# Kernel tuning notes

Hardware: AMD Instinct MI355X
Metric: run time of the kernel (lower is better)

Reference implementation:

```python
import jax, jax.numpy as jnp
import numpy as np

H = 8          # attention heads
D = 16         # per-head dim (hidden // heads)
HID = 128      # hidden_channels
OUT = 8        # out_channels of final linear
L = 2          # num_layers
NP = 100000    # num paper nodes
NA = 100000    # num author nodes
E = 500000     # edges per edge type
NEG_SLOPE = 0.2


def setup_inputs() -> dict:
    key = jax.random.key(0)
    ks = jax.random.split(key, 20)
    def nrm(k, shape, s=0.05):
        return jax.random.normal(k, shape, dtype=jnp.float32) * s
    return {
        'x_paper': jax.random.normal(ks[0], (NP, HID), dtype=jnp.float32),
        'x_author': jax.random.normal(ks[1], (NA, HID), dtype=jnp.float32),
        'Wp_p': nrm(ks[2], (L, HID, HID)),
        'bp_p': jnp.zeros((L, HID), jnp.float32),
        'Wp_a': nrm(ks[3], (L, HID, HID)),
        'bp_a': jnp.zeros((L, HID), jnp.float32),
        'as_ap': nrm(ks[4], (L, H, D), 0.2),
        'ad_ap': nrm(ks[5], (L, H, D), 0.2),
        'as_pa': nrm(ks[6], (L, H, D), 0.2),
        'ad_pa': nrm(ks[7], (L, H, D), 0.2),
        'as_pp': nrm(ks[8], (L, H, D), 0.2),
        'ad_pp': nrm(ks[9], (L, H, D), 0.2),
        'Wk': nrm(ks[10], (L, HID, HID)),
        'bk': jnp.zeros((L, HID), jnp.float32),
        'q': nrm(ks[11], (L, HID), 0.2),
        'Wout': nrm(ks[12], (HID, OUT)),
        'bout': jnp.zeros((OUT,), jnp.float32),
        'ei_ap': jax.random.randint(ks[13], (2, E), 0, NP, dtype=jnp.int32),
        'ei_pa': jax.random.randint(ks[14], (2, E), 0, NP, dtype=jnp.int32),
        'ei_pp': jax.random.randint(ks[15], (2, E), 0, NP, dtype=jnp.int32),
    }


def _leaky_relu(x):
    return jnp.where(x >= 0, x, NEG_SLOPE * x)


def _seg_softmax(alpha, dst, n):
    # PyG-style segment softmax over incoming edges of each dst node
    amax = jax.ops.segment_max(alpha, dst, num_segments=n)
    a = jnp.exp(alpha - amax[dst])
    denom = jax.ops.segment_sum(a, dst, num_segments=n) + 1e-16
    return a / denom[dst]


def _edge_attn_agg(z_src, z_dst, ei, a_s, a_d, n_dst):
    # per-edge-type GAT-style attention + scatter aggregate (HANConv message/aggregate)
    src, dst = ei[0], ei[1]
    alpha_src = (z_src * a_s).sum(-1)   # [Ns, H]
    alpha_dst = (z_dst * a_d).sum(-1)   # [Nd, H]
    alpha = _leaky_relu(alpha_src[src] + alpha_dst[dst])  # [E, H]
    alpha = _seg_softmax(alpha, dst, n_dst)
    msg = z_src[src] * alpha[:, :, None]                   # [E, H, D]
    out = jax.ops.segment_sum(msg, dst, num_segments=n_dst)
    return jax.nn.relu(out.reshape(n_dst, H * D))


def _group(outs, q, Wk, bk):
    # HANConv semantic-level attention across metapaths
    stacked = jnp.stack(outs)                               # [K, N, F]
    score = (q * jnp.tanh(stacked @ Wk + bk).mean(1)).sum(-1)  # [K]
    attn = jax.nn.softmax(score)
    return (attn[:, None, None] * stacked).sum(0)           # [N, F]


def _han_conv(xp, xa, ei_ap, ei_pa, ei_pp, Wp_p, bp_p, Wp_a, bp_a,
              as_ap, ad_ap, as_pa, ad_pa, as_pp, ad_pp, Wk, bk, q):
    zp = (xp @ Wp_p + bp_p).reshape(-1, H, D)
    za = (xa @ Wp_a + bp_a).reshape(-1, H, D)
    n_p, n_a = zp.shape[0], za.shape[0]
    out_ap = _edge_attn_agg(za, zp, ei_ap, as_ap, ad_ap, n_p)  # author -> paper
    out_pa = _edge_attn_agg(zp, za, ei_pa, as_pa, ad_pa, n_a)  # paper -> author
    out_pp = _edge_attn_agg(zp, zp, ei_pp, as_pp, ad_pp, n_p)  # paper -> paper
    new_xp = _group([out_ap, out_pp], q, Wk, bk)
    new_xa = _group([out_pa], q, Wk, bk)
    return new_xp, new_xa


def _forward(x_paper, x_author, Wp_p, bp_p, Wp_a, bp_a, as_ap, ad_ap,
             as_pa, ad_pa, as_pp, ad_pp, Wk, bk, q, Wout, bout,
             ei_ap, ei_pa, ei_pp):
    xp, xa = x_paper, x_author
    for l in range(L):
        xp, xa = _han_conv(xp, xa, ei_ap, ei_pa, ei_pp,
                           Wp_p[l], bp_p[l], Wp_a[l], bp_a[l],
                           as_ap[l], ad_ap[l], as_pa[l], ad_pa[l],
                           as_pp[l], ad_pp[l], Wk[l], bk[l], q[l])
        if l < L - 1:
            xp = jax.nn.elu(xp)  # dropout identity in eval mode (p applied only in training)
            xa = jax.nn.elu(xa)
    tgt = jax.nn.elu(xp)
    return tgt @ Wout + bout  # [NP, OUT]


def reference(x_paper, x_author, Wp_p, bp_p, Wp_a, bp_a, as_ap, ad_ap,
              as_pa, ad_pa, as_pp, ad_pp, Wk, bk, q, Wout, bout,
              ei_ap, ei_pa, ei_pp):
    return _forward(x_paper, x_author, Wp_p, bp_p, Wp_a, bp_a, as_ap, ad_ap,
                    as_pa, ad_pa, as_pp, ad_pp, Wk, bk, q, Wout, bout,
                    ei_ap, ei_pa, ei_pp)
```

## Files before the change

kernel.cpp:

```cpp
#include <hip/hip_runtime.h>

#define NHID 128
#define NHEAD 8
#define NNODE 100000
#define NEDGE 500000
#define NEG 0.2f
#define SCORE_GRID 512
#define GEMM_GRID 512
#define AGG_BLOCKS 12500
#define EB ((NEDGE + 255) / 256)
#define SB ((NNODE + 1023) / 1024)

typedef float4 f4;
typedef __attribute__((ext_vector_type(8))) short bfrag;
typedef __attribute__((ext_vector_type(4))) float facc;

__device__ inline float b2f(unsigned int u) {
    return __uint_as_float(u << 16);
}
__device__ inline unsigned short f2b(float f) {
    unsigned int u = __float_as_uint(f);
    unsigned int r = (u + 0x7FFFu + ((u >> 16) & 1u)) >> 16;
    return (unsigned short)r;
}
__device__ inline float fast_tanh(float x) {
    float e = __expf(2.f * x);
    return 1.f - 2.f / (e + 1.f);
}

struct WavSet {
    const float* W; const float* b;
    const float* v0; const float* v1; const float* v2; const float* v3;
    ushort* GT; float* bAv;
};

__global__ __launch_bounds__(256) void prep_fused(
    const float* __restrict__ w0, const float* __restrict__ w1,
    const float* __restrict__ w2, const float* __restrict__ w3,
    const float* __restrict__ w4, const float* __restrict__ w5,
    ushort* __restrict__ o0, ushort* __restrict__ o1,
    ushort* __restrict__ o2, ushort* __restrict__ o3,
    ushort* __restrict__ o4, ushort* __restrict__ o5,
    WavSet s0, WavSet s1, WavSet s2, WavSet s3,
    const int* __restrict__ e0, const int* __restrict__ e1,
    const int* __restrict__ e2, int* __restrict__ deg3)
{
    const int b = blockIdx.x;
    if (b < 384) {
        int which = b >> 6;
        int i = (b & 63) * 256 + threadIdx.x;
        const float* W = (which == 0) ? w0 : (which == 1) ? w1 : (which == 2) ? w2
                       : (which == 3) ? w3 : (which == 4) ? w4 : w5;
        ushort* Wt = (which == 0) ? o0 : (which == 1) ? o1 : (which == 2) ? o2
                   : (which == 3) ? o3 : (which == 4) ? o4 : o5;
        int fi = i >> 3, e = i & 7;
        int jk = fi >> 6, l = fi & 63;
        int j = jk >> 2, kk = jk & 3;
        int lr = l & 15, lg = l >> 4;
        Wt[i] = f2b(W[(kk * 32 + lg * 8 + e) * 128 + j * 16 + lr]);
    } else if (b < 448) {
        int bb = b - 384;
        int which = bb >> 4;
        const WavSet s = (which == 0) ? s0 : (which == 1) ? s1 : (which == 2) ? s2 : s3;
        int i = (bb & 15) * 256 + threadIdx.x;
        int fi = i >> 3, e = i & 7;
        int jk = fi >> 6, l = fi & 63;
        int jt = jk >> 2, kk = jk & 3;
        int lr = l & 15, lg = l >> 4;
        int c = jt * 16 + lr;
        int m = kk * 32 + lg * 8 + e;
        int vec = c >> 3, h = c & 7;
        const float* vp = (vec == 0) ? s.v0 : (vec == 1) ? s.v1 : (vec == 2) ? s.v2 : s.v3;
        float sv = 0.f;
        if (vp) {
            #pragma unroll
            for (int dd = 0; dd < 16; ++dd)
                sv = fmaf(s.W[m * 128 + h * 16 + dd], vp[h * 16 + dd], sv);
        }
        s.GT[i] = f2b(sv);
        if (i < 32) {
            int cc = i, vv = cc >> 3, hh = cc & 7;
            const float* vq = (vv == 0) ? s.v0 : (vv == 1) ? s.v1 : (vv == 2) ? s.v2 : s.v3;
            float t = 0.f;
            if (vq) {
                #pragma unroll
                for (int dd = 0; dd < 16; ++dd)
                    t = fmaf(s.b[hh * 16 + dd], vq[hh * 16 + dd], t);
            }
            s.bAv[cc] = t;
        }
    } else {
        int bb2 = b - 448;
        int ty = bb2 / EB, bb = bb2 % EB;
        const int* ei = (ty == 0) ? e0 : (ty == 1) ? e1 : e2;
        int e = bb * 256 + threadIdx.x;
        if (e < NEDGE) atomicAdd(deg3 + ty * NNODE + ei[NEDGE + e], 1);
    }
}

struct PArgs {
    const void* A;
    const ushort* A2;
    const ushort* WtT;
    const ushort* GT;
    const float* bias;
    const float* bAv;
    ushort* C;
    float* ao0; float* ao1; float* ao2; float* ao3;
    int mode;
};

template<int M0, int M1, int SCAT>
__global__ __launch_bounds__(256) void gemm_persist(
    PArgs g0, PArgs g1, const float* __restrict__ attn, int nt, int N,
    const int* __restrict__ e0, const int* __restrict__ e1,
    const int* __restrict__ e2, int* __restrict__ cur3, int* __restrict__ cols3)
{
    if (SCAT && blockIdx.x >= GEMM_GRID) {
        int bb2 = blockIdx.x - GEMM_GRID;
        int ty = bb2 / EB, bb = bb2 % EB;
        const int* ei = (ty == 0) ? e0 : (ty == 1) ? e1 : e2;
        int e = bb * 256 + threadIdx.x;
        if (e < NEDGE) {
            int d = ei[NEDGE + e];
            int pos = atomicAdd(cur3 + ty * NNODE + d, 1);
            cols3[ty * NEDGE + pos] = ei[e];
        }
        return;
    }

    __shared__ uint4 smem[2560];
    const int hg = GEMM_GRID >> 1;
    const int half = (blockIdx.x >= hg) ? 1 : 0;
    const PArgs ga = half ? g1 : g0;
    const int MODE = half ? M1 : M0;
    const int b0 = half ? blockIdx.x - hg : blockIdx.x;

    const int tid = threadIdx.x;
    const int l = tid & 63, w = tid >> 6;
    const int lr = l & 15, lg = l >> 4;

    {
        const uint4* ws = reinterpret_cast<const uint4*>(ga.WtT);
        const uint4* gs = reinterpret_cast<const uint4*>(ga.GT);
        #pragma unroll
        for (int i = 0; i < 8; ++i) smem[tid + i * 256] = ws[tid + i * 256];
        #pragma unroll
        for (int i = 0; i < 2; ++i) smem[2048 + tid + i * 256] = gs[tid + i * 256];
    }
    float a0 = 0.f, a1 = 0.f;
    if (MODE == 2) { a0 = attn[0]; a1 = attn[1]; }
    __syncthreads();
    const ushort* WtL = reinterpret_cast<const ushort*>(smem);
    const ushort* GL  = WtL + 16384;

    float bv[8];
    #pragma unroll
    for (int j = 0; j < 8; ++j) bv[j] = ga.bias[j * 16 + lr];
    float bA[2];
    #pragma unroll
    for (int jt = 0; jt < 2; ++jt) bA[jt] = ga.bAv[jt * 16 + lr];

    uint4 rawA[(M0 == 0 && M1 == 0) ? 8 : 16];

    auto load_raw = [&](int t) {
        const int rw0 = t * 128 + w * 32;
        #pragma unroll
        for (int i = 0; i < 2; ++i) {
            int r = rw0 + i * 16 + lr; r = (r < N) ? r : (N - 1);
            if (MODE == 1) {
                const float* ap = (const float*)ga.A + (size_t)r * 128 + lg * 8;
                #pragma unroll
                for (int kk = 0; kk < 4; ++kk) {
                    rawA[i * 8 + kk * 2]     = *reinterpret_cast<const uint4*>(ap + kk * 32);
                    rawA[i * 8 + kk * 2 + 1] = *reinterpret_cast<const uint4*>(ap + kk * 32 + 4);
                }
            } else {
                const ushort* ap = (const ushort*)ga.A + (size_t)r * 128 + lg * 8;
                #pragma unroll
                for (int kk = 0; kk < 4; ++kk)
                    rawA[i * 4 + kk] = *reinterpret_cast<const uint4*>(ap + kk * 32);
                if (MODE == 2) {
                    const ushort* ap2 = ga.A2 + (size_t)r * 128 + lg * 8;
                    #pragma unroll
                    for (int kk = 0; kk < 4; ++kk)
                        rawA[8 + i * 4 + kk] = *reinterpret_cast<const uint4*>(ap2 + kk * 32);
                }
            }
        }
    };

    if (b0 >= nt) return;
    load_raw(b0);

    for (int t = b0; t < nt; t += hg) {
        const int rw0 = t * 128 + w * 32;

        bfrag av_[2][4];
        #pragma unroll
        for (int i = 0; i < 2; ++i) {
            #pragma unroll
            for (int kk = 0; kk < 4; ++kk) {
                if (MODE == 0) {
                    av_[i][kk] = *reinterpret_cast<bfrag*>(&rawA[i * 4 + kk]);
                } else if (MODE == 1) {
                    uint4 u = rawA[i * 8 + kk * 2];
                    uint4 v = rawA[i * 8 + kk * 2 + 1];
                    bfrag fr;
                    fr[0] = (short)f2b(__uint_as_float(u.x));
                    fr[1] = (short)f2b(__uint_as_float(u.y));
                    fr[2] = (short)f2b(__uint_as_float(u.z));
                    fr[3] = (short)f2b(__uint_as_float(u.w));
                    fr[4] = (short)f2b(__uint_as_float(v.x));
                    fr[5] = (short)f2b(__uint_as_float(v.y));
                    fr[6] = (short)f2b(__uint_as_float(v.z));
                    fr[7] = (short)f2b(__uint_as_float(v.w));
                    av_[i][kk] = fr;
                } else {
                    uint4 ua = rawA[i * 4 + kk];
                    uint4 ub = rawA[8 + i * 4 + kk];
                    unsigned int aa[4] = {ua.x, ua.y, ua.z, ua.w};
                    unsigned int bb[4] = {ub.x, ub.y, ub.z, ub.w};
                    bfrag fr;
                    #pragma unroll
                    for (int q = 0; q < 4; ++q) {
                        float lo = a0 * b2f(aa[q] & 0xffffu) + a1 * b2f(bb[q] & 0xffffu);
                        float hi = a0 * b2f(aa[q] >> 16)     + a1 * b2f(bb[q] >> 16);
                        fr[q * 2]     = (short)f2b(lo);
                        fr[q * 2 + 1] = (short)f2b(hi);
                    }
                    av_[i][kk] = fr;
                }
            }
        }

        if (t + hg < nt) load_raw(t + hg);

        facc accC[2][8], accP[2][2];
        #pragma unroll
        for (int i = 0; i < 2; ++i) {
            #pragma unroll
            for (int j = 0; j < 8; ++j) accC[i][j] = (facc){0.f, 0.f, 0.f, 0.f};
            #pragma unroll
            for (int jt = 0; jt < 2; ++jt) accP[i][jt] = (facc){0.f, 0.f, 0.f, 0.f};
        }

        #pragma unroll
        for (int kk = 0; kk < 4; ++kk) {
            #pragma unroll
            for (int j = 0; j < 8; ++j) {
                bfrag bfr = *reinterpret_cast<const bfrag*>(WtL + ((j * 4 + kk) * 64 + l) * 8);
                #pragma unroll
                for (int i = 0; i < 2; ++i)
                    accC[i][j] = __builtin_amdgcn_mfma_f32_16x16x32_bf16(
                        av_[i][kk], bfr, accC[i][j], 0, 0, 0);
            }
            #pragma unroll
            for (int jt = 0; jt < 2; ++jt) {
                bfrag gfr = *reinterpret_cast<const bfrag*>(GL + ((jt * 4 + kk) * 64 + l) * 8);
                #pragma unroll
                for (int i = 0; i < 2; ++i)
                    accP[i][jt] = __builtin_amdgcn_mfma_f32_16x16x32_bf16(
                        av_[i][kk], gfr, accP[i][jt], 0, 0, 0);
            }
        }

        #pragma unroll
        for (int j = 0; j < 8; ++j) {
            #pragma unroll
            for (int i = 0; i < 2; ++i) {
                #pragma unroll
                for (int rr = 0; rr < 4; ++rr) {
                    int row = rw0 + i * 16 + lg * 4 + rr;
                    if (row < N)
                        ga.C[(size_t)row * 128 + j * 16 + lr] = f2b(accC[i][j][rr] + bv[j]);
                }
            }
        }

        #pragma unroll
        for (int jt = 0; jt < 2; ++jt) {
            int c = jt * 16 + lr;
            int vec = c >> 3, h = c & 7;
            float* ao = (vec == 0) ? ga.ao0 : (vec == 1) ? ga.ao1
                      : (vec == 2) ? ga.ao2 : ga.ao3;
            if (ao == nullptr) continue;
            #pragma unroll
            for (int i = 0; i < 2; ++i) {
                #pragma unroll
                for (int rr = 0; rr < 4; ++rr) {
                    int row = rw0 + i * 16 + lg * 4 + rr;
                    if (row < N) ao[row * 8 + h] = accP[i][jt][rr] + bA[jt];
                }
            }
        }
    }
}

__global__ __launch_bounds__(256) void score_persist(
    const ushort* __restrict__ A0, const ushort* __restrict__ A1,
    const ushort* __restrict__ WtT, const float* __restrict__ bias,
    float* __restrict__ part, int nt, int N)
{
    __shared__ uint4 smem[2048];
    __shared__ float sred[4][256];
    const int tid = threadIdx.x;
    const int l = tid & 63, w = tid >> 6;
    const int lr = l & 15, lg = l >> 4;

    {
        const uint4* ws = reinterpret_cast<const uint4*>(WtT);
        #pragma unroll
        for (int i = 0; i < 8; ++i) smem[tid + i * 256] = ws[tid + i * 256];
    }
    __syncthreads();
    const ushort* WtL = reinterpret_cast<const ushort*>(smem);

    float bv[8];
    #pragma unroll
    for (int j = 0; j < 8; ++j) bv[j] = bias[j * 16 + lr];

    float cs[2][8];
    #pragma unroll
    for (int h = 0; h < 2; ++h)
        #pragma unroll
        for (int j = 0; j < 8; ++j) cs[h][j] = 0.f;

    const int total = 2 * nt;
    for (int t = blockIdx.x; t < total; t += gridDim.x) {
        const int half = (t >= nt) ? 1 : 0;
        const ushort* A = half ? A1 : A0;
        const int bb = half ? t - nt : t;
        const int rw0 = bb * 128 + w * 32;

        bfrag av_[2][4];
        #pragma unroll
        for (int i = 0; i < 2; ++i) {
            int r = rw0 + i * 16 + lr; r = (r < N) ? r : (N - 1);
            const ushort* ap = A + (size_t)r * 128 + lg * 8;
            #pragma unroll
            for (int kk = 0; kk < 4; ++kk)
                av_[i][kk] = *reinterpret_cast<const bfrag*>(ap + kk * 32);
        }

        facc acc[2][8];
        #pragma unroll
        for (int i = 0; i < 2; ++i)
            #pragma unroll
            for (int j = 0; j < 8; ++j) acc[i][j] = (facc){0.f, 0.f, 0.f, 0.f};

        #pragma unroll
        for (int kk = 0; kk < 4; ++kk) {
            #pragma unroll
            for (int j = 0; j < 8; ++j) {
                bfrag bfr = *reinterpret_cast<const bfrag*>(WtL + ((j * 4 + kk) * 64 + l) * 8);
                #pragma unroll
                for (int i = 0; i < 2; ++i)
                    acc[i][j] = __builtin_amdgcn_mfma_f32_16x16x32_bf16(
                        av_[i][kk], bfr, acc[i][j], 0, 0, 0);
            }
        }

        #pragma unroll
        for (int j = 0; j < 8; ++j) {
            float s = 0.f;
            #pragma unroll
            for (int i = 0; i < 2; ++i) {
                #pragma unroll
                for (int r = 0; r < 4; ++r) {
                    int row = rw0 + i * 16 + lg * 4 + r;
                    if (row < N) s += fast_tanh(acc[i][j][r] + bv[j]);
                }
            }
            cs[half][j] += s;
        }
    }

    #pragma unroll
    for (int h = 0; h < 2; ++h)
        #pragma unroll
        for (int j = 0; j < 8; ++j) {
            float s = cs[h][j];
            s += __shfl_xor(s, 16, 64);
            s += __shfl_xor(s, 32, 64);
            if (lg == 0) sred[w][h * 128 + j * 16 + lr] = s;
        }
    __syncthreads();
    float tot = sred[0][tid] + sred[1][tid] + sred[2][tid] + sred[3][tid];
    part[(size_t)blockIdx.x * 256 + tid] = tot;
}

__global__ void attn_reduce(const float* __restrict__ part,
                            const float* __restrict__ qv,
                            float* __restrict__ attn, int nb)
{
    __shared__ float sm[256];
    int t = threadIdx.x;
    float s0 = 0.f, s1 = 0.f, s2 = 0.f, s3 = 0.f;
    for (int b = 0; b < nb; b += 4) {
        s0 += part[(size_t)b * 256 + t];
        s1 += part[(size_t)(b + 1) * 256 + t];
        s2 += part[(size_t)(b + 2) * 256 + t];
        s3 += part[(size_t)(b + 3) * 256 + t];
    }
    sm[t] = (s0 + s1 + s2 + s3) * qv[t & 127];
    __syncthreads();
    if (t == 0) {
        float a = 0.f, b = 0.f;
        for (int i = 0; i < 128; ++i) { a += sm[i]; b += sm[128 + i]; }
        a *= (1.0f / 100000.0f);
        b *= (1.0f / 100000.0f);
        float m = fmaxf(a, b);
        float ea = expf(a - m), eb = expf(b - m);
        float inv = 1.f / (ea + eb);
        attn[0] = ea * inv;
        attn[1] = eb * inv;
    }
}

__global__ __launch_bounds__(1024) void scan_block3(
    const int* __restrict__ deg3, int* __restrict__ offs3, int* __restrict__ bsum3)
{
    __shared__ int sd[1024];
    int ty = blockIdx.x / SB, bb = blockIdx.x % SB;
    const int* deg = deg3 + ty * NNODE;
    int* offs = offs3 + ty * (NNODE + 1);
    int t = threadIdx.x, i = bb * 1024 + t;
    int v = (i < NNODE) ? deg[i] : 0;
    sd[t] = v; __syncthreads();
    for (int o = 1; o < 1024; o <<= 1) {
        int x = (t >= o) ? sd[t - o] : 0;
        __syncthreads();
        sd[t] += x;
        __syncthreads();
    }
    if (i < NNODE) offs[i + 1] = sd[t];
    if (t == 1023) bsum3[ty * 128 + bb] = sd[t];
}

__global__ void scan_bsum3(const int* __restrict__ bsum3, int* __restrict__ boff3)
{
    int t = threadIdx.x;
    if (t < 3) {
        int run = 0;
        for (int b = 0; b < SB; ++b) { boff3[t * 128 + b] = run; run += bsum3[t * 128 + b]; }
    }
}

__global__ __launch_bounds__(1024) void scan_add3(
    int* __restrict__ offs3, const int* __restrict__ boff3, int* __restrict__ cur3)
{
    int ty = blockIdx.x / SB, bb = blockIdx.x % SB;
    int* offs = offs3 + ty * (NNODE + 1);
    int* cur = cur3 + ty * NNODE;
    int i = bb * 1024 + threadIdx.x;
    if (i == 0) { offs[0] = 0; cur[0] = 0; }
    if (i < NNODE) {
        int v = offs[i + 1] + boff3[ty * 128 + bb];
        offs[i + 1] = v;
        if (i + 1 < NNODE) cur[i + 1] = v;
    }
}

struct AggJob {
    const int* offs; const int* cols;
    const float* asrc; const float* adst;
    const ushort* z; ushort* out;
};

__global__ __launch_bounds__(256) void agg_multi(AggJob j0, AggJob j1, AggJob j2)
{
    int jb = blockIdx.x / AGG_BLOCKS;
    const AggJob jj = (jb == 0) ? j0 : (jb == 1) ? j1 : j2;
    int bb = blockIdx.x - jb * AGG_BLOCKS;
    int w = threadIdx.x >> 6;
    int lane = threadIdx.x & 63;
    int halfid = lane >> 5;
    int sl = lane & 31;
    int d = bb * 8 + w * 2 + halfid;
    int h = sl >> 2;
    float ad = jj.adst[d * 8 + h];
    int e0 = jj.offs[d], e1 = jj.offs[d + 1];
    float acc0 = 0.f, acc1 = 0.f, acc2 = 0.f, acc3 = 0.f, psum = 0.f;
    const ushort* zbase = jj.z + sl * 4;
    for (int base = e0; base < e1; base += 4) {
        int idx[4];
        #pragma unroll
        for (int i = 0; i < 4; ++i) {
            int ee = base + i;
            idx[i] = jj.cols[(ee < e1) ? ee : (e1 - 1)];
        }
        float xs[4];
        #pragma unroll
        for (int i = 0; i < 4; ++i) xs[i] = jj.asrc[idx[i] * 8 + h];
        uint2 zv[4];
        #pragma unroll
        for (int i = 0; i < 4; ++i)
            zv[i] = *reinterpret_cast<const uint2*>(zbase + (size_t)idx[i] * 128);
        #pragma unroll
        for (int i = 0; i < 4; ++i) {
            float a = xs[i] + ad;
            a = fmaxf(a, NEG * a);
            float p = __expf(a);
            p = (base + i < e1) ? p : 0.f;
            acc0 = fmaf(p, b2f(zv[i].x & 0xffffu), acc0);
            acc1 = fmaf(p, b2f(zv[i].x >> 16),     acc1);
            acc2 = fmaf(p, b2f(zv[i].y & 0xffffu), acc2);
            acc3 = fmaf(p, b2f(zv[i].y >> 16),     acc3);
            psum += p;
        }
    }
    float inv = 1.f / (psum + 1e-16f);
    uint2 pk;
    pk.x = (unsigned int)f2b(fmaxf(acc0 * inv, 0.f))
         | ((unsigned int)f2b(fmaxf(acc1 * inv, 0.f)) << 16);
    pk.y = (unsigned int)f2b(fmaxf(acc2 * inv, 0.f))
         | ((unsigned int)f2b(fmaxf(acc3 * inv, 0.f)) << 16);
    *reinterpret_cast<uint2*>(jj.out + (size_t)d * 128 + sl * 4) = pk;
}

__global__ __launch_bounds__(256) void final_gemm_mix(
    const ushort* __restrict__ XA_, const ushort* __restrict__ XB_,
    const float* __restrict__ attn, const float* __restrict__ W,
    const float* __restrict__ bias, float* __restrict__ out, int N)
{
    __shared__ float Ws[128][8];
    __shared__ __align__(16) float Xs[32][129];
    int tid = threadIdx.x;
    float a0 = attn[0], a1 = attn[1];
    for (int i = tid; i < 1024; i += 256) Ws[i >> 3][i & 7] = W[i];
    int row0 = blockIdx.x * 32;
    for (int i = tid; i < 512; i += 256) {
        int r = i >> 4, q = i & 15;
        int gr = row0 + r;
        uint4 va = make_uint4(0, 0, 0, 0), vb = make_uint4(0, 0, 0, 0);
        if (gr < N) {
            va = reinterpret_cast<const uint4*>(XA_ + (size_t)gr * 128)[q];
            vb = reinterpret_cast<const uint4*>(XB_ + (size_t)gr * 128)[q];
        }
        int c = q * 8;
        unsigned int ua[4] = {va.x, va.y, va.z, va.w};
        unsigned int ub[4] = {vb.x, vb.y, vb.z, vb.w};
        #pragma unroll
        for (int qq = 0; qq < 4; ++qq) {
            Xs[r][c + qq * 2]     = a0 * b2f(ua[qq] & 0xffffu) + a1 * b2f(ub[qq] & 0xffffu);
            Xs[r][c + qq * 2 + 1] = a0 * b2f(ua[qq] >> 16)     + a1 * b2f(ub[qq] >> 16);
        }
    }
    __syncthreads();
    int r = tid >> 3, o = tid & 7;
    int gr = row0 + r;
    if (gr < N) {
        float s = bias[o];
        #pragma unroll
        for (int k = 0; k < 128; ++k) s = fmaf(Xs[r][k], Ws[k][o], s);
        out[(size_t)gr * 8 + o] = s;
    }
}

extern "C" void kernel_launch(void* const* d_in, const int* in_sizes, int n_in,
                              void* d_out, int out_size, void* d_ws, size_t ws_size,
                              hipStream_t stream) {
    const float* x_paper  = (const float*)d_in[0];
    const float* x_author = (const float*)d_in[1];
    const float* Wp_p = (const float*)d_in[2];
    const float* bp_p = (const float*)d_in[3];
    const float* Wp_a = (const float*)d_in[4];
    const float* bp_a = (const float*)d_in[5];
    const float* as_ap = (const float*)d_in[6];
    const float* ad_ap = (const float*)d_in[7];
    const float* as_pa = (const float*)d_in[8];
    const float* ad_pa = (const float*)d_in[9];
    const float* as_pp = (const float*)d_in[10];
    const float* ad_pp = (const float*)d_in[11];
    const float* Wk   = (const float*)d_in[12];
    const float* bk   = (const float*)d_in[13];
    const float* qv   = (const float*)d_in[14];
    const float* Wout = (const float*)d_in[15];
    const float* bout = (const float*)d_in[16];
    const int* ei_ap = (const int*)d_in[17];
    const int* ei_pa = (const int*)d_in[18];
    const int* ei_pp = (const int*)d_in[19];

    const size_t NB = (size_t)NNODE * 128;
    ushort* Z0 = (ushort*)d_ws;
    ushort* Z1 = Z0 + NB;
    ushort* Z2 = Z1 + NB;
    ushort* Z3 = Z2 + NB;
    ushort* P0 = Z3 + NB;
    ushort* P1 = P0 + NB;
    float* fp = (float*)(P1 + NB);
    float* ap_s = fp; fp += NNODE * 8;
    float* ap_d = fp; fp += NNODE * 8;
    float* pa_s = fp; fp += NNODE * 8;
    float* pa_d = fp; fp += NNODE * 8;
    float* pp_s = fp; fp += NNODE * 8;
    float* pp_d = fp; fp += NNODE * 8;
    float* part = fp; fp += (size_t)SCORE_GRID * 256;
    float* attn = fp; fp += 16;
    float* bAv_p0 = fp; fp += 32;
    float* bAv_a0 = fp; fp += 32;
    float* bAv_p1 = fp; fp += 32;
    float* bAv_a1 = fp; fp += 32;
    ushort* up = (ushort*)fp;
    ushort* WtP0 = up; up += 16384;
    ushort* WtA0 = up; up += 16384;
    ushort* WtP1 = up; up += 16384;
    ushort* WtA1 = up; up += 16384;
    ushort* WtK0 = up; up += 16384;
    ushort* WtK1 = up; up += 16384;
    ushort* G_p0 = up; up += 4096;
    ushort* G_a0 = up; up += 4096;
    ushort* G_p1 = up; up += 4096;
    ushort* G_a1 = up; up += 4096;
    int* ip = (int*)(((size_t)up + 15) & ~(size_t)15);
    int* cols3 = ip; ip += 3 * NEDGE;
    int* offs3 = ip; ip += 3 * (NNODE + 1);
    int* deg3  = ip; ip += 3 * NNODE;
    int* cur3  = ip; ip += 3 * NNODE;
    int* bsum3 = ip; ip += 3 * 128;
    int* boff3 = ip; ip += 3 * 128;

    const int* cols_ap = cols3;
    const int* cols_pa = cols3 + NEDGE;
    const int* cols_pp = cols3 + 2 * NEDGE;
    const int* offs_ap = offs3;
    const int* offs_pa = offs3 + (NNODE + 1);
    const int* offs_pp = offs3 + 2 * (NNODE + 1);

    const dim3 blk(256);
    const int nt128 = (NNODE + 127) / 128;
    const int wo = 128 * 128, bo = 128, ao = 128;

    hipMemsetAsync(deg3, 0, 3 * NNODE * 4, stream);
    {
        WavSet s0{Wp_p, bp_p, ad_ap, as_pa, as_pp, ad_pp, G_p0, bAv_p0};
        WavSet s1{Wp_a, bp_a, as_ap, ad_pa, nullptr, nullptr, G_a0, bAv_a0};
        WavSet s2{Wp_p + wo, bp_p + bo, ad_ap + ao, as_pp + ao, ad_pp + ao, nullptr, G_p1, bAv_p1};
        WavSet s3{Wp_a + wo, bp_a + bo, as_ap + ao, nullptr, nullptr, nullptr, G_a1, bAv_a1};
        prep_fused<<<448 + 3 * EB, blk, 0, stream>>>(
            Wp_p, Wp_a, Wp_p + wo, Wp_a + wo, Wk, Wk + wo,
            WtP0, WtA0, WtP1, WtA1, WtK0, WtK1,
            s0, s1, s2, s3, ei_ap, ei_pa, ei_pp, deg3);
    }
    scan_block3<<<3 * SB, 1024, 0, stream>>>(deg3, offs3, bsum3);
    scan_bsum3<<<1, 64, 0, stream>>>(bsum3, boff3);
    scan_add3<<<3 * SB, 1024, 0, stream>>>(offs3, boff3, cur3);

    {
        PArgs gp{x_paper,  nullptr, WtP0, G_p0, bp_p, bAv_p0, Z0, ap_d, pa_s, pp_s, pp_d, 1};
        PArgs ga{x_author, nullptr, WtA0, G_a0, bp_a, bAv_a0, Z1, ap_s, pa_d, nullptr, nullptr, 1};
        gemm_persist<1, 1, 1><<<GEMM_GRID + 3 * EB, blk, 0, stream>>>(
            gp, ga, attn, nt128, NNODE, ei_ap, ei_pa, ei_pp, cur3, cols3);
    }

    {
        AggJob a0{offs_ap, cols_ap, ap_s, ap_d, Z1, Z2};
        AggJob a1{offs_pa, cols_pa, pa_s, pa_d, Z0, Z3};
        AggJob a2{offs_pp, cols_pp, pp_s, pp_d, Z0, P0};
        agg_multi<<<3 * AGG_BLOCKS, blk, 0, stream>>>(a0, a1, a2);
    }

    score_persist<<<SCORE_GRID, blk, 0, stream>>>(Z2, P0, WtK0, bk, part, nt128, NNODE);
    attn_reduce<<<1, 256, 0, stream>>>(part, qv, attn, SCORE_GRID);

    {
        PArgs gp{Z2, P0, WtP1, G_p1, bp_p + bo, bAv_p1, Z0, ap_d, pp_s, pp_d, nullptr, 2};
        PArgs ga{Z3, nullptr, WtA1, G_a1, bp_a + bo, bAv_a1, Z1, ap_s, nullptr, nullptr, nullptr, 0};
        gemm_persist<2, 0, 0><<<GEMM_GRID, blk, 0, stream>>>(
            gp, ga, attn, nt128, NNODE, nullptr, nullptr, nullptr, nullptr, nullptr);
    }

    {
        AggJob a0{offs_ap, cols_ap, ap_s, ap_d, Z1, Z2};
        AggJob a1{offs_pp, cols_pp, pp_s, pp_d, Z0, P1};
        agg_multi<<<2 * AGG_BLOCKS, blk, 0, stream>>>(a0, a1, a1);
    }

    score_persist<<<SCORE_GRID, blk, 0, stream>>>(Z2, P1, WtK1, bk + bo, part, nt128, NNODE);
    attn_reduce<<<1, 256, 0, stream>>>(part, qv + bo, attn, SCORE_GRID);

    final_gemm_mix<<<(NNODE + 31) / 32, blk, 0, stream>>>(Z2, P1, attn, Wout, bout, (float*)d_out, NNODE);
}
```

Baseline: 532.4 us.

## Pre-convert input features to bf16 in prep kernel and fold block-sum scan

Input paper/author features are converted from fp32 to bf16 inside the prep kernel, writing into scratch buffers, so the first-layer GEMM runs in bf16 mode (mode 0) and reads half the bytes per tile. The separate single-thread block-offset scan kernel is removed; each scan_add3 block now sums the preceding block totals itself, which saves a launch. CSR column writes become nontemporal stores. The conversion adds an extra full read of the fp32 inputs plus a bf16 write, so total traffic may not drop; the gain relies on shrinking the GEMM's load phase and on the launch saved.

```diff
diff --git a/kernel.cpp b/kernel.cpp
--- a/kernel.cpp
+++ b/kernel.cpp
@@ -10,6 +10,7 @@
 #define AGG_BLOCKS 12500
 #define EB ((NEDGE + 255) / 256)
 #define SB ((NNODE + 1023) / 1024)
+#define CVTB 6250
 
 typedef float4 f4;
 typedef __attribute__((ext_vector_type(8))) short bfrag;
@@ -43,7 +44,9 @@
     ushort* __restrict__ o4, ushort* __restrict__ o5,
     WavSet s0, WavSet s1, WavSet s2, WavSet s3,
     const int* __restrict__ e0, const int* __restrict__ e1,
-    const int* __restrict__ e2, int* __restrict__ deg3)
+    const int* __restrict__ e2, int* __restrict__ deg3,
+    const float* __restrict__ xp_f, const float* __restrict__ xa_f,
+    ushort* __restrict__ XP, ushort* __restrict__ XA)
 {
     const int b = blockIdx.x;
     if (b < 384) {
@@ -89,12 +92,23 @@
             }
             s.bAv[cc] = t;
         }
-    } else {
+    } else if (b < 448 + 3 * EB) {
         int bb2 = b - 448;
         int ty = bb2 / EB, bb = bb2 % EB;
         const int* ei = (ty == 0) ? e0 : (ty == 1) ? e1 : e2;
         int e = bb * 256 + threadIdx.x;
         if (e < NEDGE) atomicAdd(deg3 + ty * NNODE + ei[NEDGE + e], 1);
+    } else {
+        int bb2 = b - 448 - 3 * EB;
+        const float* src = (bb2 < CVTB) ? xp_f : xa_f;
+        ushort* dst = (bb2 < CVTB) ? XP : XA;
+        int i = (bb2 % CVTB) * 256 + threadIdx.x;
+        size_t off = (size_t)i * 8;
+        f4 u = *reinterpret_cast<const f4*>(src + off);
+        f4 v = *reinterpret_cast<const f4*>(src + off + 4);
+        ushort rs[8] = {f2b(u.x), f2b(u.y), f2b(u.z), f2b(u.w),
+                        f2b(v.x), f2b(v.y), f2b(v.z), f2b(v.w)};
+        *reinterpret_cast<uint4*>(dst + off) = *reinterpret_cast<uint4*>(rs);
     }
 }
 
@@ -124,7 +138,7 @@
         if (e < NEDGE) {
             int d = ei[NEDGE + e];
             int pos = atomicAdd(cur3 + ty * NNODE + d, 1);
-            cols3[ty * NEDGE + pos] = ei[e];
+            __builtin_nontemporal_store(ei[e], cols3 + (size_t)ty * NEDGE + pos);
         }
         return;
     }
@@ -161,7 +175,7 @@
     #pragma unroll
     for (int jt = 0; jt < 2; ++jt) bA[jt] = ga.bAv[jt * 16 + lr];
 
-    uint4 rawA[(M0 == 0 && M1 == 0) ? 8 : 16];
+    uint4 rawA[(M0 <= 0 && M1 <= 0) ? 8 : 16];
 
     auto load_raw = [&](int t) {
         const int rw0 = t * 128 + w * 32;
@@ -438,25 +452,24 @@
     if (t == 1023) bsum3[ty * 128 + bb] = sd[t];
 }
 
-__global__ void scan_bsum3(const int* __restrict__ bsum3, int* __restrict__ boff3)
-{
-    int t = threadIdx.x;
-    if (t < 3) {
+__global__ __launch_bounds__(1024) void scan_add3(
+    int* __restrict__ offs3, const int* __restrict__ bsum3, int* __restrict__ cur3)
+{
+    __shared__ int spref;
+    int ty = blockIdx.x / SB, bb = blockIdx.x % SB;
+    if (threadIdx.x == 0) {
         int run = 0;
-        for (int b = 0; b < SB; ++b) { boff3[t * 128 + b] = run; run += bsum3[t * 128 + b]; }
-    }
-}
-
-__global__ __launch_bounds__(1024) void scan_add3(
-    int* __restrict__ offs3, const int* __restrict__ boff3, int* __restrict__ cur3)
-{
-    int ty = blockIdx.x / SB, bb = blockIdx.x % SB;
+        for (int b = 0; b < bb; ++b) run += bsum3[ty * 128 + b];
+        spref = run;
+    }
+    __syncthreads();
+    int boff = spref;
     int* offs = offs3 + ty * (NNODE + 1);
     int* cur = cur3 + ty * NNODE;
     int i = bb * 1024 + threadIdx.x;
     if (i == 0) { offs[0] = 0; cur[0] = 0; }
     if (i < NNODE) {
-        int v = offs[i + 1] + boff3[ty * 128 + bb];
+        int v = offs[i + 1] + boff;
         offs[i + 1] = v;
         if (i + 1 < NNODE) cur[i + 1] = v;
     }
@@ -589,6 +602,8 @@
     ushort* Z3 = Z2 + NB;
     ushort* P0 = Z3 + NB;
     ushort* P1 = P0 + NB;
+    ushort* XP = P1;
+    ushort* XA = Z2;
     float* fp = (float*)(P1 + NB);
     float* ap_s = fp; fp += NNODE * 8;
     float* ap_d = fp; fp += NNODE * 8;
@@ -619,7 +634,6 @@
     int* deg3  = ip; ip += 3 * NNODE;
     int* cur3  = ip; ip += 3 * NNODE;
     int* bsum3 = ip; ip += 3 * 128;
-    int* boff3 = ip; ip += 3 * 128;
 
     const int* cols_ap = cols3;
     const int* cols_pa = cols3 + NEDGE;
@@ -638,19 +652,19 @@
         WavSet s1{Wp_a, bp_a, as_ap, ad_pa, nullptr, nullptr, G_a0, bAv_a0};
         WavSet s2{Wp_p + wo, bp_p + bo, ad_ap + ao, as_pp + ao, ad_pp + ao, nullptr, G_p1, bAv_p1};
         WavSet s3{Wp_a + wo, bp_a + bo, as_ap + ao, nullptr, nullptr, nullptr, G_a1, bAv_a1};
-        prep_fused<<<448 + 3 * EB, blk, 0, stream>>>(
+        prep_fused<<<448 + 3 * EB + 2 * CVTB, blk, 0, stream>>>(
             Wp_p, Wp_a, Wp_p + wo, Wp_a + wo, Wk, Wk + wo,
             WtP0, WtA0, WtP1, WtA1, WtK0, WtK1,
-            s0, s1, s2, s3, ei_ap, ei_pa, ei_pp, deg3);
+            s0, s1, s2, s3, ei_ap, ei_pa, ei_pp, deg3,
+            x_paper, x_author, XP, XA);
     }
     scan_block3<<<3 * SB, 1024, 0, stream>>>(deg3, offs3, bsum3);
-    scan_bsum3<<<1, 64, 0, stream>>>(bsum3, boff3);
-    scan_add3<<<3 * SB, 1024, 0, stream>>>(offs3, boff3, cur3);
+    scan_add3<<<3 * SB, 1024, 0, stream>>>(offs3, bsum3, cur3);
 
     {
-        PArgs gp{x_paper,  nullptr, WtP0, G_p0, bp_p, bAv_p0, Z0, ap_d, pa_s, pp_s, pp_d, 1};
-        PArgs ga{x_author, nullptr, WtA0, G_a0, bp_a, bAv_a0, Z1, ap_s, pa_d, nullptr, nullptr, 1};
-        gemm_persist<1, 1, 1><<<GEMM_GRID + 3 * EB, blk, 0, stream>>>(
+        PArgs gp{XP, nullptr, WtP0, G_p0, bp_p, bAv_p0, Z0, ap_d, pa_s, pp_s, pp_d, 0};
+        PArgs ga{XA, nullptr, WtA0, G_a0, bp_a, bAv_a0, Z1, ap_s, pa_d, nullptr, nullptr, 0};
+        gemm_persist<0, 0, 1><<<GEMM_GRID + 3 * EB, blk, 0, stream>>>(
             gp, ga, attn, nt128, NNODE, ei_ap, ei_pa, ei_pp, cur3, cols3);
     }
 
```

Result: slower. 551.7 us (+3.6%).
